# Kernel tuning notes

Hardware: AMD Instinct MI355X
Metric: run time of the kernel (lower is better)

## Reference

```python
import jax, jax.numpy as jnp
import numpy as np


def _elu_plus_one(x):
    # F.elu(x) + 1 == exp(x) for x<0, x+1 for x>=0
    return jnp.where(x > 0, x + 1.0, jnp.exp(jnp.minimum(x, 0.0)))


def setup_inputs() -> dict:
    key = jax.random.key(0)
    kq, kk, kv = jax.random.split(key, 3)
    B, N, D = 16, 8192, 64
    q = jax.random.normal(kq, (B, N, D), dtype=jnp.float32)
    k = jax.random.normal(kk, (B, N, D), dtype=jnp.float32)
    v = jax.random.normal(kv, (B, N, D), dtype=jnp.float32)
    return {"q": q, "k": k, "v": v}


def reference(q, k, v):
    # linear attention with elu+1 feature map:
    # out = phi(q) @ (phi(k)^T @ v) / (D * N)
    qf = _elu_plus_one(q)          # [B, N, D]
    kf = _elu_plus_one(k)          # [B, N, D]
    kv = jnp.einsum('bnd,bne->bde', kf, v)   # [B, D, D] small intermediate
    denom = jnp.asarray(v.shape[-1] * v.shape[-2], dtype=v.dtype)
    out = jnp.einsum('bnd,bde->bne', qf, kv) / denom  # [B, N, D]
    return out
```

## Files before the change

### kernel.cpp

```cpp
#include <hip/hip_runtime.h>

#define B_ 16
#define N_ 8192
#define D_ 64

__device__ __forceinline__ float elu1(float x) {
    return x > 0.0f ? x + 1.0f : __expf(x);
}

template <int TI>
__global__ __launch_bounds__(256) void k1_partial(const float* __restrict__ kin,
                                                  const float* __restrict__ vin,
                                                  float* __restrict__ part,
                                                  int C, int R) {
    const int bid = blockIdx.x;
    const int b = bid / C, c = bid % C;
    const size_t base = ((size_t)b * N_ + (size_t)c * R) * D_;
    const float4* kp = (const float4*)(kin + base);
    const float4* vp = (const float4*)(vin + base);

    __shared__ float lk[TI][D_];
    __shared__ float lv[TI][D_];

    const int tid = threadIdx.x;
    const int td = tid >> 4;
    const int te = tid & 15;

    float acc[4][4];
#pragma unroll
    for (int i = 0; i < 4; ++i)
#pragma unroll
        for (int j = 0; j < 4; ++j) acc[i][j] = 0.0f;

    const int ntiles = R / TI;
    for (int t = 0; t < ntiles; ++t) {
#pragma unroll
        for (int u = tid; u < TI * (D_ / 4); u += 256) {
            float4 kk = kp[t * TI * (D_ / 4) + u];
            float4 vv = vp[t * TI * (D_ / 4) + u];
            const int r = u >> 4, cc = (u & 15) * 4;
            float4 ek;
            ek.x = elu1(kk.x); ek.y = elu1(kk.y);
            ek.z = elu1(kk.z); ek.w = elu1(kk.w);
            *(float4*)&lk[r][cc] = ek;
            *(float4*)&lv[r][cc] = vv;
        }
        __syncthreads();
#pragma unroll 8
        for (int r = 0; r < TI; ++r) {
            const float4 kk = *(const float4*)&lk[r][td * 4];
            const float4 vv = *(const float4*)&lv[r][te * 4];
            const float kd[4] = {kk.x, kk.y, kk.z, kk.w};
            const float ve[4] = {vv.x, vv.y, vv.z, vv.w};
#pragma unroll
            for (int i = 0; i < 4; ++i)
#pragma unroll
                for (int j = 0; j < 4; ++j)
                    acc[i][j] = __fmaf_rn(kd[i], ve[j], acc[i][j]);
        }
        __syncthreads();
    }

    float* pb = part + (size_t)bid * (D_ * D_);
#pragma unroll
    for (int i = 0; i < 4; ++i) {
        float4 o = {acc[i][0], acc[i][1], acc[i][2], acc[i][3]};
        *(float4*)&pb[(4 * td + i) * D_ + 4 * te] = o;
    }
}

template <int TI>
__global__ __launch_bounds__(256) void k1_atomic(const float* __restrict__ kin,
                                                 const float* __restrict__ vin,
                                                 float* __restrict__ kv,
                                                 int C, int R) {
    const int bid = blockIdx.x;
    const int b = bid / C, c = bid % C;
    const size_t base = ((size_t)b * N_ + (size_t)c * R) * D_;
    const float4* kp = (const float4*)(kin + base);
    const float4* vp = (const float4*)(vin + base);

    __shared__ float lk[TI][D_];
    __shared__ float lv[TI][D_];

    const int tid = threadIdx.x;
    const int td = tid >> 4;
    const int te = tid & 15;

    float acc[4][4];
#pragma unroll
    for (int i = 0; i < 4; ++i)
#pragma unroll
        for (int j = 0; j < 4; ++j) acc[i][j] = 0.0f;

    const int ntiles = R / TI;
    for (int t = 0; t < ntiles; ++t) {
#pragma unroll
        for (int u = tid; u < TI * (D_ / 4); u += 256) {
            float4 kk = kp[t * TI * (D_ / 4) + u];
            float4 vv = vp[t * TI * (D_ / 4) + u];
            const int r = u >> 4, cc = (u & 15) * 4;
            float4 ek;
            ek.x = elu1(kk.x); ek.y = elu1(kk.y);
            ek.z = elu1(kk.z); ek.w = elu1(kk.w);
            *(float4*)&lk[r][cc] = ek;
            *(float4*)&lv[r][cc] = vv;
        }
        __syncthreads();
#pragma unroll 8
        for (int r = 0; r < TI; ++r) {
            const float4 kk = *(const float4*)&lk[r][td * 4];
            const float4 vv = *(const float4*)&lv[r][te * 4];
            const float kd[4] = {kk.x, kk.y, kk.z, kk.w};
            const float ve[4] = {vv.x, vv.y, vv.z, vv.w};
#pragma unroll
            for (int i = 0; i < 4; ++i)
#pragma unroll
                for (int j = 0; j < 4; ++j)
                    acc[i][j] = __fmaf_rn(kd[i], ve[j], acc[i][j]);
        }
        __syncthreads();
    }

    float* pb = kv + (size_t)b * (D_ * D_);
#pragma unroll
    for (int i = 0; i < 4; ++i)
#pragma unroll
        for (int j = 0; j < 4; ++j)
            atomicAdd(&pb[(4 * td + i) * D_ + 4 * te + j], acc[i][j]);
}

__global__ __launch_bounds__(256) void k2_reduce(float* __restrict__ part, int C) {
    const int i = blockIdx.x * 256 + threadIdx.x;
    const int b = i >> 12, j = i & 4095;
    float* p = part + (size_t)b * C * (D_ * D_) + j;
    float s = 0.0f;
    for (int c = 0; c < C; ++c) s += p[(size_t)c * (D_ * D_)];
    p[0] = s;
}

__global__ __launch_bounds__(256) void k3_out(const float* __restrict__ q,
                                              const float* __restrict__ kvbuf,
                                              size_t kvstride,
                                              float* __restrict__ out) {
    const int bpb = N_ / 256;
    const int b = blockIdx.x / bpb;
    const int n0 = (blockIdx.x % bpb) * 256;

    __shared__ float skv[D_ * D_];
    const float4* kp = (const float4*)(kvbuf + (size_t)b * kvstride);
#pragma unroll
    for (int u = threadIdx.x; u < (D_ * D_) / 4; u += 256)
        *(float4*)&skv[u * 4] = kp[u];
    __syncthreads();

    const size_t row = (size_t)b * N_ + n0 + threadIdx.x;
    const float4* qp = (const float4*)(q + row * D_);

    float qf[D_];
#pragma unroll
    for (int j = 0; j < D_ / 4; ++j) {
        float4 t = qp[j];
        qf[4 * j + 0] = elu1(t.x);
        qf[4 * j + 1] = elu1(t.y);
        qf[4 * j + 2] = elu1(t.z);
        qf[4 * j + 3] = elu1(t.w);
    }

    float acc[D_];
#pragma unroll
    for (int e = 0; e < D_; ++e) acc[e] = 0.0f;

#pragma unroll 4
    for (int d = 0; d < D_; ++d) {
        const float qd = qf[d];
#pragma unroll
        for (int e4 = 0; e4 < D_ / 4; ++e4) {
            const float4 kvv = *(const float4*)&skv[d * D_ + e4 * 4];
            acc[4 * e4 + 0] = __fmaf_rn(qd, kvv.x, acc[4 * e4 + 0]);
            acc[4 * e4 + 1] = __fmaf_rn(qd, kvv.y, acc[4 * e4 + 1]);
            acc[4 * e4 + 2] = __fmaf_rn(qd, kvv.z, acc[4 * e4 + 2]);
            acc[4 * e4 + 3] = __fmaf_rn(qd, kvv.w, acc[4 * e4 + 3]);
        }
    }

    const float scale = 1.0f / (float)((size_t)D_ * N_);
    float4* op = (float4*)(out + row * D_);
#pragma unroll
    for (int j = 0; j < D_ / 4; ++j) {
        float4 o = {acc[4 * j + 0] * scale, acc[4 * j + 1] * scale,
                    acc[4 * j + 2] * scale, acc[4 * j + 3] * scale};
        op[j] = o;
    }
}

extern "C" void kernel_launch(void* const* d_in, const int* in_sizes, int n_in,
                              void* d_out, int out_size, void* d_ws, size_t ws_size,
                              hipStream_t stream) {
    const float* q = (const float*)d_in[0];
    const float* k = (const float*)d_in[1];
    const float* v = (const float*)d_in[2];
    float* out = (float*)d_out;
    float* ws = (float*)d_ws;

    const size_t mat = (size_t)D_ * D_;

    int C = 0;
    for (int cc = 64; cc >= 2; cc >>= 1) {
        if (ws_size >= (size_t)B_ * cc * mat * sizeof(float)) { C = cc; break; }
    }

    if (C >= 2) {
        const int R = N_ / C;
        k1_partial<32><<<B_ * C, 256, 0, stream>>>(k, v, ws, C, R);
        k2_reduce<<<(int)(B_ * mat) / 256, 256, 0, stream>>>(ws, C);
        k3_out<<<B_ * (N_ / 256), 256, 0, stream>>>(q, ws, (size_t)C * mat, out);
    } else {
        hipMemsetAsync(d_ws, 0, B_ * mat * sizeof(float), stream);
        const int C2 = 64, R = N_ / C2;
        k1_atomic<32><<<B_ * C2, 256, 0, stream>>>(k, v, ws, C2, R);
        k3_out<<<B_ * (N_ / 256), 256, 0, stream>>>(q, ws, mat, out);
    }
}
```

Measured before the change: 208.4 us.

## Rework kv partial kernel with shuffles and retile output kernel per row quarter

The partial k^T v kernel now has each wave own a slice of rows and an 8x8 register tile. Rows are exchanged with wave shuffles instead of staged through shared memory, and the four waves' partial sums are combined in LDS before one write per block. The output kernel assigns four threads per row, each owning 16 output columns, with q features broadcast by shuffle. This cuts per-thread registers and raises occupancy compared with the previous 64-accumulator-per-thread layout. The reduction kernel also splits its sum into four independent accumulators for more memory-level parallelism.

```diff
diff --git a/kernel.cpp b/kernel.cpp
--- a/kernel.cpp
+++ b/kernel.cpp
@@ -8,65 +8,84 @@
     return x > 0.0f ? x + 1.0f : __expf(x);
 }
 
-template <int TI>
-__global__ __launch_bounds__(256) void k1_partial(const float* __restrict__ kin,
-                                                  const float* __restrict__ vin,
-                                                  float* __restrict__ part,
-                                                  int C, int R) {
+__global__ __launch_bounds__(256, 4) void k1_partial(const float* __restrict__ kin,
+                                                     const float* __restrict__ vin,
+                                                     float* __restrict__ part,
+                                                     int C, int R) {
     const int bid = blockIdx.x;
     const int b = bid / C, c = bid % C;
-    const size_t base = ((size_t)b * N_ + (size_t)c * R) * D_;
-    const float4* kp = (const float4*)(kin + base);
-    const float4* vp = (const float4*)(vin + base);
-
-    __shared__ float lk[TI][D_];
-    __shared__ float lv[TI][D_];
-
-    const int tid = threadIdx.x;
-    const int td = tid >> 4;
-    const int te = tid & 15;
-
-    float acc[4][4];
-#pragma unroll
-    for (int i = 0; i < 4; ++i)
-#pragma unroll
-        for (int j = 0; j < 4; ++j) acc[i][j] = 0.0f;
-
-    const int ntiles = R / TI;
-    for (int t = 0; t < ntiles; ++t) {
-#pragma unroll
-        for (int u = tid; u < TI * (D_ / 4); u += 256) {
-            float4 kk = kp[t * TI * (D_ / 4) + u];
-            float4 vv = vp[t * TI * (D_ / 4) + u];
-            const int r = u >> 4, cc = (u & 15) * 4;
-            float4 ek;
-            ek.x = elu1(kk.x); ek.y = elu1(kk.y);
-            ek.z = elu1(kk.z); ek.w = elu1(kk.w);
-            *(float4*)&lk[r][cc] = ek;
-            *(float4*)&lv[r][cc] = vv;
+    const int w = threadIdx.x >> 6;
+    const int lane = threadIdx.x & 63;
+    const int dq = lane >> 3;
+    const int eq = lane & 7;
+
+    const int rows_per_wave = R >> 2;
+    const size_t rowbase = (size_t)b * N_ + (size_t)c * R + (size_t)w * rows_per_wave;
+    const float4* kp = (const float4*)(kin + rowbase * D_);
+    const float4* vp = (const float4*)(vin + rowbase * D_);
+
+    float acc[8][8];
+#pragma unroll
+    for (int i = 0; i < 8; ++i)
+#pragma unroll
+        for (int jj = 0; jj < 8; ++jj) acc[i][jj] = 0.0f;
+
+    const int ngroups = rows_per_wave >> 2;
+    for (int g = 0; g < ngroups; ++g) {
+        float4 k4 = kp[g * 64 + lane];
+        float4 v4 = vp[g * 64 + lane];
+        k4.x = elu1(k4.x); k4.y = elu1(k4.y); k4.z = elu1(k4.z); k4.w = elu1(k4.w);
+        const float ka[4] = {k4.x, k4.y, k4.z, k4.w};
+        const float va[4] = {v4.x, v4.y, v4.z, v4.w};
+
+#pragma unroll
+        for (int rr = 0; rr < 4; ++rr) {
+            const int sk0 = rr * 16 + 2 * dq;
+            const int sv0 = rr * 16 + 2 * eq;
+            float kk[8], vv[8];
+#pragma unroll
+            for (int cc = 0; cc < 4; ++cc) {
+                kk[cc]     = __shfl(ka[cc], sk0,     64);
+                kk[cc + 4] = __shfl(ka[cc], sk0 + 1, 64);
+                vv[cc]     = __shfl(va[cc], sv0,     64);
+                vv[cc + 4] = __shfl(va[cc], sv0 + 1, 64);
+            }
+#pragma unroll
+            for (int i = 0; i < 8; ++i)
+#pragma unroll
+                for (int jj = 0; jj < 8; ++jj)
+                    acc[i][jj] = __fmaf_rn(kk[i], vv[jj], acc[i][jj]);
+        }
+    }
+
+    __shared__ float red[D_ * D_];
+    for (int ww = 0; ww < 4; ++ww) {
+        if (w == ww) {
+#pragma unroll
+            for (int i = 0; i < 8; ++i)
+#pragma unroll
+                for (int jq = 0; jq < 2; ++jq) {
+                    float* p = &red[(8 * dq + i) * D_ + 8 * eq + 4 * jq];
+                    if (ww == 0) {
+                        float4 o = {acc[i][4 * jq + 0], acc[i][4 * jq + 1],
+                                    acc[i][4 * jq + 2], acc[i][4 * jq + 3]};
+                        *(float4*)p = o;
+                    } else {
+                        float4 cur = *(const float4*)p;
+                        float4 o = {cur.x + acc[i][4 * jq + 0], cur.y + acc[i][4 * jq + 1],
+                                    cur.z + acc[i][4 * jq + 2], cur.w + acc[i][4 * jq + 3]};
+                        *(float4*)p = o;
+                    }
+                }
         }
         __syncthreads();
-#pragma unroll 8
-        for (int r = 0; r < TI; ++r) {
-            const float4 kk = *(const float4*)&lk[r][td * 4];
-            const float4 vv = *(const float4*)&lv[r][te * 4];
-            const float kd[4] = {kk.x, kk.y, kk.z, kk.w};
-            const float ve[4] = {vv.x, vv.y, vv.z, vv.w};
-#pragma unroll
-            for (int i = 0; i < 4; ++i)
-#pragma unroll
-                for (int j = 0; j < 4; ++j)
-                    acc[i][j] = __fmaf_rn(kd[i], ve[j], acc[i][j]);
-        }
-        __syncthreads();
-    }
-
-    float* pb = part + (size_t)bid * (D_ * D_);
-#pragma unroll
-    for (int i = 0; i < 4; ++i) {
-        float4 o = {acc[i][0], acc[i][1], acc[i][2], acc[i][3]};
-        *(float4*)&pb[(4 * td + i) * D_ + 4 * te] = o;
-    }
+    }
+
+    float4* pb = (float4*)(part + (size_t)bid * (D_ * D_));
+    const float4* rp = (const float4*)red;
+#pragma unroll
+    for (int u = 0; u < 4; ++u)
+        pb[threadIdx.x + 256 * u] = rp[threadIdx.x + 256 * u];
 }
 
 template <int TI>
@@ -132,65 +151,78 @@
 
 __global__ __launch_bounds__(256) void k2_reduce(float* __restrict__ part, int C) {
     const int i = blockIdx.x * 256 + threadIdx.x;
-    const int b = i >> 12, j = i & 4095;
-    float* p = part + (size_t)b * C * (D_ * D_) + j;
-    float s = 0.0f;
-    for (int c = 0; c < C; ++c) s += p[(size_t)c * (D_ * D_)];
-    p[0] = s;
-}
-
-__global__ __launch_bounds__(256) void k3_out(const float* __restrict__ q,
-                                              const float* __restrict__ kvbuf,
-                                              size_t kvstride,
-                                              float* __restrict__ out) {
-    const int bpb = N_ / 256;
-    const int b = blockIdx.x / bpb;
-    const int n0 = (blockIdx.x % bpb) * 256;
-
+    const int b = i >> 12, jj = i & 4095;
+    float* p = part + (size_t)b * C * (D_ * D_) + jj;
+    float s0 = 0.0f, s1 = 0.0f, s2 = 0.0f, s3 = 0.0f;
+    int c = 0;
+    for (; c + 4 <= C; c += 4) {
+        s0 += p[(size_t)(c + 0) * (D_ * D_)];
+        s1 += p[(size_t)(c + 1) * (D_ * D_)];
+        s2 += p[(size_t)(c + 2) * (D_ * D_)];
+        s3 += p[(size_t)(c + 3) * (D_ * D_)];
+    }
+    for (; c < C; ++c) s0 += p[(size_t)c * (D_ * D_)];
+    p[0] = (s0 + s1) + (s2 + s3);
+}
+
+__global__ __launch_bounds__(256, 4) void k3_out(const float* __restrict__ q,
+                                                 const float* __restrict__ kvbuf,
+                                                 int kvstride,
+                                                 float* __restrict__ out) {
     __shared__ float skv[D_ * D_];
-    const float4* kp = (const float4*)(kvbuf + (size_t)b * kvstride);
-#pragma unroll
-    for (int u = threadIdx.x; u < (D_ * D_) / 4; u += 256)
-        *(float4*)&skv[u * 4] = kp[u];
+    const int b = blockIdx.x >> 7;
+    const int tile = blockIdx.x & 127;
+
+    const float4* kvg = (const float4*)(kvbuf + (size_t)b * kvstride);
+    float4* skv4 = (float4*)skv;
+#pragma unroll
+    for (int u = 0; u < 4; ++u)
+        skv4[threadIdx.x + 256 * u] = kvg[threadIdx.x + 256 * u];
+
+    const int r = threadIdx.x >> 2;
+    const int j = threadIdx.x & 3;
+    const size_t row = (size_t)b * N_ + (size_t)tile * 64 + r;
+
+    const float4* qp = (const float4*)(q + row * D_ + j * 16);
+    float qf[16];
+#pragma unroll
+    for (int u = 0; u < 4; ++u) {
+        float4 t = qp[u];
+        qf[4 * u + 0] = elu1(t.x);
+        qf[4 * u + 1] = elu1(t.y);
+        qf[4 * u + 2] = elu1(t.z);
+        qf[4 * u + 3] = elu1(t.w);
+    }
     __syncthreads();
 
-    const size_t row = (size_t)b * N_ + n0 + threadIdx.x;
-    const float4* qp = (const float4*)(q + row * D_);
-
-    float qf[D_];
-#pragma unroll
-    for (int j = 0; j < D_ / 4; ++j) {
-        float4 t = qp[j];
-        qf[4 * j + 0] = elu1(t.x);
-        qf[4 * j + 1] = elu1(t.y);
-        qf[4 * j + 2] = elu1(t.z);
-        qf[4 * j + 3] = elu1(t.w);
-    }
-
-    float acc[D_];
-#pragma unroll
-    for (int e = 0; e < D_; ++e) acc[e] = 0.0f;
-
-#pragma unroll 4
-    for (int d = 0; d < D_; ++d) {
-        const float qd = qf[d];
-#pragma unroll
-        for (int e4 = 0; e4 < D_ / 4; ++e4) {
-            const float4 kvv = *(const float4*)&skv[d * D_ + e4 * 4];
-            acc[4 * e4 + 0] = __fmaf_rn(qd, kvv.x, acc[4 * e4 + 0]);
-            acc[4 * e4 + 1] = __fmaf_rn(qd, kvv.y, acc[4 * e4 + 1]);
-            acc[4 * e4 + 2] = __fmaf_rn(qd, kvv.z, acc[4 * e4 + 2]);
-            acc[4 * e4 + 3] = __fmaf_rn(qd, kvv.w, acc[4 * e4 + 3]);
+    float4 acc[4];
+#pragma unroll
+    for (int s = 0; s < 4; ++s) acc[s] = {0.0f, 0.0f, 0.0f, 0.0f};
+
+    for (int d0 = 0; d0 < 4; ++d0) {
+        const int dbase = d0 * 16;
+#pragma unroll
+        for (int dd = 0; dd < 16; ++dd) {
+            const float qd = __shfl(qf[dd], d0, 4);
+            const int d = dbase + dd;
+#pragma unroll
+            for (int s = 0; s < 4; ++s) {
+                const float4 kvv = *(const float4*)&skv[d * D_ + s * 16 + j * 4];
+                acc[s].x = __fmaf_rn(qd, kvv.x, acc[s].x);
+                acc[s].y = __fmaf_rn(qd, kvv.y, acc[s].y);
+                acc[s].z = __fmaf_rn(qd, kvv.z, acc[s].z);
+                acc[s].w = __fmaf_rn(qd, kvv.w, acc[s].w);
+            }
         }
     }
 
     const float scale = 1.0f / (float)((size_t)D_ * N_);
     float4* op = (float4*)(out + row * D_);
 #pragma unroll
-    for (int j = 0; j < D_ / 4; ++j) {
-        float4 o = {acc[4 * j + 0] * scale, acc[4 * j + 1] * scale,
-                    acc[4 * j + 2] * scale, acc[4 * j + 3] * scale};
-        op[j] = o;
+    for (int s = 0; s < 4; ++s) {
+        float4 o = {acc[s].x * scale, acc[s].y * scale,
+                    acc[s].z * scale, acc[s].w * scale};
+        op[s * 4 + j] = o;
     }
 }
 
@@ -212,13 +244,13 @@
 
     if (C >= 2) {
         const int R = N_ / C;
-        k1_partial<32><<<B_ * C, 256, 0, stream>>>(k, v, ws, C, R);
+        k1_partial<<<B_ * C, 256, 0, stream>>>(k, v, ws, C, R);
         k2_reduce<<<(int)(B_ * mat) / 256, 256, 0, stream>>>(ws, C);
-        k3_out<<<B_ * (N_ / 256), 256, 0, stream>>>(q, ws, (size_t)C * mat, out);
+        k3_out<<<B_ * (N_ / 64), 256, 0, stream>>>(q, ws, (int)(C * mat), out);
     } else {
         hipMemsetAsync(d_ws, 0, B_ * mat * sizeof(float), stream);
         const int C2 = 64, R = N_ / C2;
         k1_atomic<32><<<B_ * C2, 256, 0, stream>>>(k, v, ws, C2, R);
-        k3_out<<<B_ * (N_ / 256), 256, 0, stream>>>(q, ws, mat, out);
-    }
-}
+        k3_out<<<B_ * (N_ / 64), 256, 0, stream>>>(q, ws, (int)mat, out);
+    }
+}
```

Measured after the change: 175.5 us. -15.8%, faster.
